# Kernel tuning notes

Hardware: AMD Instinct MI355X
Metric: run time of the kernel (lower is better)

The kernel has to match this reference:

```python
import jax, jax.numpy as jnp
import numpy as np

N = 50000   # nodes
E = 600000  # directed edges
B = 128     # graphs
IN = 128
H = 128
K = 30      # sort-pool k
C_OUT = 32
KER = 5
OUT_DIM = 10
L_OUT = K - KER + 1  # 26


def setup_inputs() -> dict:
    key = jax.random.key(0)
    ks = jax.random.split(key, 12)
    s = 0.05
    return {
        "x": jax.random.normal(ks[0], (N, IN), jnp.float32),
        "edge_index": jax.random.randint(ks[1], (2, E), 0, N),
        "batch": jnp.sort(jax.random.randint(ks[2], (N,), 0, B)),
        "W0": jax.random.normal(ks[3], (IN, H), jnp.float32) * s,
        "b0": jnp.zeros((H,), jnp.float32),
        "W1": jax.random.normal(ks[4], (H, H), jnp.float32) * s,
        "b1": jnp.zeros((H,), jnp.float32),
        "W2": jax.random.normal(ks[5], (H, H), jnp.float32) * s,
        "b2": jnp.zeros((H,), jnp.float32),
        "conv_w": jax.random.normal(ks[6], (C_OUT, H, KER), jnp.float32) * s,
        "conv_b": jnp.zeros((C_OUT,), jnp.float32),
        "lin1_w": jax.random.normal(ks[7], (C_OUT * L_OUT, H), jnp.float32) * s,
        "lin1_b": jnp.zeros((H,), jnp.float32),
        "lin2_w": jax.random.normal(ks[8], (H, OUT_DIM), jnp.float32) * s,
        "lin2_b": jnp.zeros((OUT_DIM,), jnp.float32),
    }


def reference(x, edge_index, batch, W0, b0, W1, b1, W2, b2,
              conv_w, conv_b, lin1_w, lin1_b, lin2_w, lin2_b):
    # --- GCN normalization (A + I, symmetric deg^-1/2) ---
    loops = jnp.arange(N)
    row = jnp.concatenate([edge_index[0], loops])  # source
    col = jnp.concatenate([edge_index[1], loops])  # target (aggregation side)
    deg = jax.ops.segment_sum(jnp.ones_like(col, dtype=x.dtype), col, num_segments=N)
    dinv = jax.lax.rsqrt(jnp.maximum(deg, 1.0))
    norm = dinv[row] * dinv[col]  # [E+N]

    def gcn(h, W, b):
        hw = h @ W                                            # [N,H]
        msg = hw[row] * norm[:, None]                         # gather [E+N,H]
        return jax.ops.segment_sum(msg, col, num_segments=N) + b

    h = jax.nn.relu(gcn(x, W0, b0))
    h = jax.nn.relu(gcn(h, W1, b1))
    h = jax.nn.relu(gcn(h, W2, b2))

    # --- SortAggregation: per-graph sort by last channel (desc), top-K, zero-pad ---
    last = h[:, -1]
    order = jnp.lexsort((-last, batch))  # primary: batch, secondary: last desc
    hs = h[order]
    bs = batch[order]
    counts = jax.ops.segment_sum(jnp.ones((N,), jnp.int32), batch, num_segments=B)
    starts = jnp.cumsum(counts) - counts  # exclusive prefix sum
    rank = jnp.arange(N) - starts[bs]     # within-graph rank after sort
    r = jnp.where(rank < K, rank, K)      # overflow bucket K is discarded
    pooled = jnp.zeros((B, K + 1, H), h.dtype).at[bs, r].add(hs)[:, :K]  # [B,K,H]

    # --- conv1d head (NCH layout, matches torch view/transpose) ---
    xc = jnp.transpose(pooled, (0, 2, 1))  # [B,H,K]
    y = jax.lax.conv_general_dilated(xc, conv_w, (1,), "VALID",
                                     dimension_numbers=("NCH", "OIH", "NCH"))
    y = jax.nn.relu(y + conv_b[None, :, None])  # [B,C_OUT,L_OUT]
    y = y.reshape(B, -1)
    y = jax.nn.relu(y @ lin1_w + lin1_b)
    return y @ lin2_w + lin2_b  # [B,OUT_DIM]
```

## Files before the change

kernel.cpp:

```cpp
#include <hip/hip_runtime.h>
#include <math.h>

#define Nn 50000
#define Ee 600000
#define Bg 128
#define Hd 128
#define Kt 30
#define CO 32
#define KW 5
#define LOUT 26
#define CAP 2048
#define SCB 196
#define MMB 782

typedef float v2f __attribute__((ext_vector_type(2)));
typedef short bf16x8 __attribute__((ext_vector_type(8)));
typedef float f32x4 __attribute__((ext_vector_type(4)));

__device__ __forceinline__ unsigned short bfr(float v) {
    unsigned u = __builtin_bit_cast(unsigned, v);
    unsigned r = (u + 0x7FFFu + ((u >> 16) & 1u)) >> 16;
    return (unsigned short)r;
}
__device__ __forceinline__ float bff(unsigned short h) {
    unsigned u = ((unsigned)h) << 16;
    return __builtin_bit_cast(float, u);
}

__global__ void countpack_kernel(const int* __restrict__ ei, const int* __restrict__ batch,
                            int* __restrict__ deg_i, int* __restrict__ bstart,
                            const float* __restrict__ conv_w, float* __restrict__ wT2,
                            const float* __restrict__ W0, const float* __restrict__ W1,
                            const float* __restrict__ W2,
                            ushort* __restrict__ Bph, ushort* __restrict__ Bpm,
                            ushort* __restrict__ Bpl) {
    int i = blockIdx.x * 256 + threadIdx.x;
    if (i < Ee) atomicAdd(&deg_i[ei[Ee + i]], 1);
    if (i < Nn) {
        int b = batch[i];
        if (i == 0) bstart[b] = 0;
        else if (batch[i - 1] != b) bstart[b] = i;
    }
    if (i == 0) bstart[Bg] = Nn;
    if (i < CO * KW * Hd) {
        int ci = i & 127;
        int r = i >> 7;
        int o = r / KW, k = r - o * KW;
        wT2[i] = conv_w[((size_t)o * Hd + ci) * KW + k];
    }
    if (i < 3 * 2048) {
        int l = i >> 11;
        int r = i & 2047;
        int kc = r >> 9;
        int n = (r >> 6) & 7;
        int lane = r & 63;
        int m = lane & 15, kq = lane >> 4;
        const float* W = (l == 0) ? W0 : (l == 1) ? W1 : W2;
        int col = n * 16 + m;
        size_t off = ((size_t)l * 2048 + (size_t)((kc * 8 + n) * 64 + lane)) * 8;
#pragma unroll
        for (int j = 0; j < 8; ++j) {
            float v = W[(size_t)(kc * 32 + kq * 8 + j) * Hd + col];
            unsigned short h = bfr(v);
            float r1 = v - bff(h);
            unsigned short mid = bfr(r1);
            Bph[off + j] = h;
            Bpm[off + j] = mid;
            Bpl[off + j] = bfr(r1 - bff(mid));
        }
    }
}

__global__ __launch_bounds__(256) void scanBC2_kernel(const int* __restrict__ deg_i,
                            int* __restrict__ row_ptr, float* __restrict__ dinv,
                            int* __restrict__ bstart) {
    __shared__ int ls[256];
    __shared__ int boffS;
    int tid = threadIdx.x;
    int b = blockIdx.x;
    int s = 0;
    for (int k = 0; k < b; ++k)
        s += deg_i[k * 256 + tid] + 1;
    ls[tid] = s;
    __syncthreads();
    for (int off = 128; off > 0; off >>= 1) {
        if (tid < off) ls[tid] += ls[tid + off];
        __syncthreads();
    }
    if (tid == 0) boffS = ls[0];
    __syncthreads();
    int boff = boffS;
    int i = b * 256 + tid;
    int v2 = 0;
    if (i < Nn) {
        int raw = deg_i[i];
        v2 = raw + 1;
        dinv[i] = 1.0f / sqrtf((float)(raw + 2));
    }
    ls[tid] = v2;
    __syncthreads();
    for (int off = 1; off < 256; off <<= 1) {
        int t = (tid >= off) ? ls[tid - off] : 0;
        __syncthreads();
        ls[tid] += t;
        __syncthreads();
    }
    if (i < Nn) row_ptr[i + 1] = ls[tid] + boff;
    if (i == 0) row_ptr[0] = 0;
    if (b == 0 && tid == 0) {
        for (int bb = Bg - 1; bb >= 0; --bb)
            if (bstart[bb] == -1) bstart[bb] = bstart[bb + 1];
    }
}

__device__ __forceinline__ void mmx_body(int bid, int tid,
                            const float* __restrict__ Hin,
                            const ushort* __restrict__ Bph, const ushort* __restrict__ Bpm,
                            const ushort* __restrict__ Bpl,
                            const float* __restrict__ dinv, float* __restrict__ hw) {
    int w = tid >> 6, lane = tid & 63;
    int m = lane & 15, kq = lane >> 4;
    int rowA = bid * 64 + w * 16 + m;
    bool va = rowA < Nn;
    const float* ap = Hin + (size_t)rowA * Hd;
    f32x4 acc[8];
#pragma unroll
    for (int n = 0; n < 8; ++n) acc[n] = (f32x4)0.f;
#pragma unroll
    for (int kc = 0; kc < 4; ++kc) {
        bf16x8 a0 = (bf16x8)0, a1 = (bf16x8)0, a2 = (bf16x8)0;
        if (va) {
            float av[8];
            *(float4*)&av[0] = *(const float4*)(ap + kc * 32 + kq * 8);
            *(float4*)&av[4] = *(const float4*)(ap + kc * 32 + kq * 8 + 4);
#pragma unroll
            for (int j = 0; j < 8; ++j) {
                unsigned short h = bfr(av[j]);
                float r1 = av[j] - bff(h);
                unsigned short mid = bfr(r1);
                a0[j] = (short)h;
                a1[j] = (short)mid;
                a2[j] = (short)bfr(r1 - bff(mid));
            }
        }
        const ushort* bhp = Bph + (size_t)((kc * 8) * 64 + lane) * 8;
        const ushort* bmp = Bpm + (size_t)((kc * 8) * 64 + lane) * 8;
        const ushort* blp = Bpl + (size_t)((kc * 8) * 64 + lane) * 8;
#pragma unroll
        for (int n = 0; n < 8; ++n) {
            bf16x8 b0 = *(const bf16x8*)(bhp + (size_t)n * 64 * 8);
            bf16x8 b1 = *(const bf16x8*)(bmp + (size_t)n * 64 * 8);
            bf16x8 b2 = *(const bf16x8*)(blp + (size_t)n * 64 * 8);
            acc[n] = __builtin_amdgcn_mfma_f32_16x16x32_bf16(a0, b0, acc[n], 0, 0, 0);
            acc[n] = __builtin_amdgcn_mfma_f32_16x16x32_bf16(a1, b0, acc[n], 0, 0, 0);
            acc[n] = __builtin_amdgcn_mfma_f32_16x16x32_bf16(a0, b1, acc[n], 0, 0, 0);
            acc[n] = __builtin_amdgcn_mfma_f32_16x16x32_bf16(a1, b1, acc[n], 0, 0, 0);
            acc[n] = __builtin_amdgcn_mfma_f32_16x16x32_bf16(a2, b0, acc[n], 0, 0, 0);
            acc[n] = __builtin_amdgcn_mfma_f32_16x16x32_bf16(a0, b2, acc[n], 0, 0, 0);
        }
    }
    int rbase = bid * 64 + w * 16 + kq * 4;
#pragma unroll
    for (int reg = 0; reg < 4; ++reg) {
        int r = rbase + reg;
        if (r < Nn) {
            float s = dinv[r];
#pragma unroll
            for (int n = 0; n < 8; ++n)
                hw[(size_t)r * Hd + n * 16 + m] = acc[n][reg] * s;
        }
    }
}

__global__ __launch_bounds__(256) void mmx_kernel(const float* __restrict__ Hin,
                            const ushort* __restrict__ Bph, const ushort* __restrict__ Bpm,
                            const ushort* __restrict__ Bpl,
                            const float* __restrict__ dinv, float* __restrict__ hw) {
    mmx_body(blockIdx.x, threadIdx.x, Hin, Bph, Bpm, Bpl, dinv, hw);
}

__global__ __launch_bounds__(256) void mmxfill_kernel(const float* __restrict__ Hin,
                            const ushort* __restrict__ Bph, const ushort* __restrict__ Bpm,
                            const ushort* __restrict__ Bpl,
                            const float* __restrict__ dinv, float* __restrict__ hw,
                            const int* __restrict__ ei, const int* __restrict__ row_ptr,
                            int* __restrict__ cnt, int* __restrict__ csr_src) {
    if (blockIdx.x < MMB) {
        mmx_body(blockIdx.x, threadIdx.x, Hin, Bph, Bpm, Bpl, dinv, hw);
    } else {
        int e = (blockIdx.x - MMB) * 256 + threadIdx.x;
        if (e < Ee) {
            int c = ei[Ee + e];
            int r = ei[e];
            int p = row_ptr[c] + atomicAdd(&cnt[c], 1) + 1;
            csr_src[p] = r;
        }
    }
}

__global__ __launch_bounds__(256) void agg_kernel(const float* __restrict__ hw,
                            const int* __restrict__ row_ptr, const int* __restrict__ csr_src,
                            const float* __restrict__ dinv, const float* __restrict__ bias,
                            float* __restrict__ hout) {
    int node = blockIdx.x * 4 + (threadIdx.x >> 6);
    if (node >= Nn) return;
    int lane = threadIdx.x & 63;
    const v2f* hw2 = (const v2f*)hw;
    v2f a0 = hw2[(size_t)node * 64 + lane];
    v2f a1 = 0.f, a2 = 0.f, a3 = 0.f;
    v2f a4 = 0.f, a5 = 0.f, a6 = 0.f, a7 = 0.f;
    int e0 = row_ptr[node], e1 = row_ptr[node + 1];
    int e = e0;
    for (; e + 7 < e1; e += 8) {
        int s0 = __builtin_nontemporal_load(csr_src + e);
        int s1 = __builtin_nontemporal_load(csr_src + e + 1);
        int s2 = __builtin_nontemporal_load(csr_src + e + 2);
        int s3 = __builtin_nontemporal_load(csr_src + e + 3);
        int s4 = __builtin_nontemporal_load(csr_src + e + 4);
        int s5 = __builtin_nontemporal_load(csr_src + e + 5);
        int s6 = __builtin_nontemporal_load(csr_src + e + 6);
        int s7 = __builtin_nontemporal_load(csr_src + e + 7);
        a0 += hw2[(size_t)s0 * 64 + lane];
        a1 += hw2[(size_t)s1 * 64 + lane];
        a2 += hw2[(size_t)s2 * 64 + lane];
        a3 += hw2[(size_t)s3 * 64 + lane];
        a4 += hw2[(size_t)s4 * 64 + lane];
        a5 += hw2[(size_t)s5 * 64 + lane];
        a6 += hw2[(size_t)s6 * 64 + lane];
        a7 += hw2[(size_t)s7 * 64 + lane];
    }
    if (e + 3 < e1) {
        int s0 = __builtin_nontemporal_load(csr_src + e);
        int s1 = __builtin_nontemporal_load(csr_src + e + 1);
        int s2 = __builtin_nontemporal_load(csr_src + e + 2);
        int s3 = __builtin_nontemporal_load(csr_src + e + 3);
        a4 += hw2[(size_t)s0 * 64 + lane];
        a5 += hw2[(size_t)s1 * 64 + lane];
        a6 += hw2[(size_t)s2 * 64 + lane];
        a7 += hw2[(size_t)s3 * 64 + lane];
        e += 4;
    }
    for (; e < e1; ++e) {
        int s0 = __builtin_nontemporal_load(csr_src + e);
        a0 += hw2[(size_t)s0 * 64 + lane];
    }
    v2f acc = ((a0 + a1) + (a2 + a3)) + ((a4 + a5) + (a6 + a7));
    float d = dinv[node];
    v2f bv = ((const v2f*)bias)[lane];
    v2f o;
    o.x = fmaxf(fmaf(d, acc.x, bv.x), 0.f);
    o.y = fmaxf(fmaf(d, acc.y, bv.y), 0.f);
    ((v2f*)hout)[(size_t)node * 64 + lane] = o;
}

__global__ __launch_bounds__(1024) void tail_kernel(const float* __restrict__ h,
                            const int* __restrict__ bstart,
                            const float* __restrict__ wT2, const float* __restrict__ conv_b,
                            const float* __restrict__ l1w, const float* __restrict__ l1b,
                            const float* __restrict__ l2w, const float* __restrict__ l2b,
                            float* __restrict__ out) {
    __shared__ float vals[CAP];
    __shared__ float xcl[Kt][130];
    __shared__ float fl[CO * LOUT];
    __shared__ float pz[8][Hd];
    __shared__ float z[Hd];
    __shared__ int selS[Kt];
    int b = blockIdx.x, tid = threadIdx.x;

    int s0 = bstart[b], s1 = bstart[b + 1];
    int n = s1 - s0;
    int nc = n < CAP ? n : CAP;
    if (tid < Kt) selS[tid] = -1;
    for (int j = tid; j < nc; j += 1024)
        vals[j] = h[(size_t)(s0 + j) * Hd + (Hd - 1)];
    __syncthreads();

    for (int j = tid; j < nc; j += 1024) {
        float vj = vals[j];
        int rank = 0;
        for (int i = 0; i < nc; ++i) {
            float vi = vals[i];
            rank += (vi > vj || (vi == vj && i < j)) ? 1 : 0;
        }
        if (rank < Kt) selS[rank] = s0 + j;
    }
    __syncthreads();

    for (int i = tid; i < Kt * Hd; i += 1024) {
        int t = i >> 7, c = i & 127;
        int s = selS[t];
        xcl[t][c] = (s >= 0) ? h[(size_t)s * Hd + c] : 0.f;
    }
    __syncthreads();
    if (tid < CO * LOUT) {
        int o = tid / LOUT, t = tid - o * LOUT;
        float acc = conv_b[o];
#pragma unroll
        for (int k = 0; k < KW; ++k) {
            const float* xr = &xcl[t + k][0];
            const float* wr = wT2 + ((size_t)o * KW + k) * Hd;
#pragma unroll 8
            for (int c4 = 0; c4 < 32; ++c4) {
                float2 xa = *(const float2*)(xr + c4 * 4);
                float2 xb = *(const float2*)(xr + c4 * 4 + 2);
                float4 wv = *(const float4*)(wr + c4 * 4);
                acc = fmaf(xa.x, wv.x, acc);
                acc = fmaf(xa.y, wv.y, acc);
                acc = fmaf(xb.x, wv.z, acc);
                acc = fmaf(xb.y, wv.w, acc);
            }
        }
        fl[tid] = fmaxf(acc, 0.f);
    }
    __syncthreads();
    int hh = tid & 127, chunk = tid >> 7;
    int m0 = chunk * 104;
    float acc = 0.f;
    const float* lw = l1w + (size_t)m0 * Hd + hh;
#pragma unroll 8
    for (int m = 0; m < 104; ++m)
        acc = fmaf(fl[m0 + m], lw[(size_t)m * Hd], acc);
    pz[chunk][hh] = acc;
    __syncthreads();
    if (tid < Hd) {
        float a = l1b[tid];
#pragma unroll
        for (int q = 0; q < 8; ++q) a += pz[q][tid];
        z[tid] = fmaxf(a, 0.f);
    }
    __syncthreads();
    if (tid < 10) {
        float a2 = l2b[tid];
        for (int j = 0; j < Hd; ++j)
            a2 = fmaf(z[j], l2w[j * 10 + tid], a2);
        out[b * 10 + tid] = a2;
    }
}

extern "C" void kernel_launch(void* const* d_in, const int* in_sizes, int n_in,
                              void* d_out, int out_size, void* d_ws, size_t ws_size,
                              hipStream_t stream) {
    const float* x      = (const float*)d_in[0];
    const int*   ei     = (const int*)d_in[1];
    const int*   batch  = (const int*)d_in[2];
    const float* W0     = (const float*)d_in[3];
    const float* b0     = (const float*)d_in[4];
    const float* W1     = (const float*)d_in[5];
    const float* b1     = (const float*)d_in[6];
    const float* W2     = (const float*)d_in[7];
    const float* b2     = (const float*)d_in[8];
    const float* conv_w = (const float*)d_in[9];
    const float* conv_b = (const float*)d_in[10];
    const float* l1w    = (const float*)d_in[11];
    const float* l1b    = (const float*)d_in[12];
    const float* l2w    = (const float*)d_in[13];
    const float* l2b    = (const float*)d_in[14];
    float* out = (float*)d_out;

    int* wsI = (int*)d_ws;
    size_t off = 0;
    int*   deg_i   = wsI + off; off += Nn;
    int*   cnt     = wsI + off; off += Nn;
    int*   bstart  = wsI + off; off += 132;
    int*   row_ptr = wsI + off; off += 50004;
    float* dinv    = (float*)(wsI + off); off += Nn;
    int*   csr_src = wsI + off; off += Ee;
    off = (off + 3) & ~(size_t)3;
    ushort* Bph  = (ushort*)(wsI + off); off += 3 * 16384 / 2;
    ushort* Bpm  = (ushort*)(wsI + off); off += 3 * 16384 / 2;
    ushort* Bpl  = (ushort*)(wsI + off); off += 3 * 16384 / 2;
    float* hw    = (float*)(wsI + off); off += (size_t)Nn * Hd;
    float* hbuf  = (float*)(wsI + off); off += (size_t)Nn * Hd;
    float* wT2   = (float*)(wsI + off); off += CO * KW * Hd;

    hipMemsetAsync(deg_i, 0xFF, (size_t)(Nn + Nn + 132) * 4, stream);
    countpack_kernel<<<(Ee + 255) / 256, 256, 0, stream>>>(ei, batch, deg_i, bstart,
        conv_w, wT2, W0, W1, W2, Bph, Bpm, Bpl);
    scanBC2_kernel<<<SCB, 256, 0, stream>>>(deg_i, row_ptr, dinv, bstart);
    dim3 aggGrid((Nn + 3) / 4);
    mmxfill_kernel<<<MMB + (Ee + 255) / 256, 256, 0, stream>>>(x, Bph, Bpm, Bpl,
        dinv, hw, ei, row_ptr, cnt, csr_src);
    agg_kernel<<<aggGrid, 256, 0, stream>>>(hw, row_ptr, csr_src, dinv, b0, hbuf);
    mmx_kernel<<<MMB, 256, 0, stream>>>(hbuf, Bph + 16384, Bpm + 16384, Bpl + 16384, dinv, hw);
    agg_kernel<<<aggGrid, 256, 0, stream>>>(hw, row_ptr, csr_src, dinv, b1, hbuf);
    mmx_kernel<<<MMB, 256, 0, stream>>>(hbuf, Bph + 32768, Bpm + 32768, Bpl + 32768, dinv, hw);
    agg_kernel<<<aggGrid, 256, 0, stream>>>(hw, row_ptr, csr_src, dinv, b2, hbuf);
    tail_kernel<<<Bg, 1024, 0, stream>>>(hbuf, bstart, wT2, conv_b,
                                         l1w, l1b, l2w, l2b, out);
}
```

Baseline: 443.3 us.

## Compute only last channel for all nodes, full aggregation only for top-K

The final full-width aggregation over all nodes is replaced by a lightweight kernel that aggregates only channel 127, which is the sort key. The tail kernel then runs the full 128-channel aggregation only for the 30 selected nodes per graph. This avoids gathering and writing the whole N×H tensor for the last layer. In exchange, the last-column gather is strided (one float per 512-byte row, so poor coalescing) and the tail does serial per-node aggregation. Results must match those of the old full aggregation for both ranking and features.

```diff
diff --git a/kernel.cpp b/kernel.cpp
--- a/kernel.cpp
+++ b/kernel.cpp
@@ -253,8 +253,57 @@
     ((v2f*)hout)[(size_t)node * 64 + lane] = o;
 }
 
-__global__ __launch_bounds__(1024) void tail_kernel(const float* __restrict__ h,
-                            const int* __restrict__ bstart,
+__global__ __launch_bounds__(256) void lastcol_kernel(const float* __restrict__ hw,
+                            const int* __restrict__ row_ptr, const int* __restrict__ csr_src,
+                            const float* __restrict__ dinv, const float* __restrict__ b2,
+                            float* __restrict__ lastv) {
+    int node = blockIdx.x * 256 + threadIdx.x;
+    if (node >= Nn) return;
+    float a0 = hw[(size_t)node * Hd + 127];
+    float a1 = 0.f, a2 = 0.f, a3 = 0.f, a4 = 0.f, a5 = 0.f, a6 = 0.f, a7 = 0.f;
+    int e0 = row_ptr[node], e1 = row_ptr[node + 1];
+    int e = e0;
+    for (; e + 7 < e1; e += 8) {
+        int s0 = __builtin_nontemporal_load(csr_src + e);
+        int s1 = __builtin_nontemporal_load(csr_src + e + 1);
+        int s2 = __builtin_nontemporal_load(csr_src + e + 2);
+        int s3 = __builtin_nontemporal_load(csr_src + e + 3);
+        int s4 = __builtin_nontemporal_load(csr_src + e + 4);
+        int s5 = __builtin_nontemporal_load(csr_src + e + 5);
+        int s6 = __builtin_nontemporal_load(csr_src + e + 6);
+        int s7 = __builtin_nontemporal_load(csr_src + e + 7);
+        a0 += hw[(size_t)s0 * Hd + 127];
+        a1 += hw[(size_t)s1 * Hd + 127];
+        a2 += hw[(size_t)s2 * Hd + 127];
+        a3 += hw[(size_t)s3 * Hd + 127];
+        a4 += hw[(size_t)s4 * Hd + 127];
+        a5 += hw[(size_t)s5 * Hd + 127];
+        a6 += hw[(size_t)s6 * Hd + 127];
+        a7 += hw[(size_t)s7 * Hd + 127];
+    }
+    if (e + 3 < e1) {
+        int s0 = __builtin_nontemporal_load(csr_src + e);
+        int s1 = __builtin_nontemporal_load(csr_src + e + 1);
+        int s2 = __builtin_nontemporal_load(csr_src + e + 2);
+        int s3 = __builtin_nontemporal_load(csr_src + e + 3);
+        a4 += hw[(size_t)s0 * Hd + 127];
+        a5 += hw[(size_t)s1 * Hd + 127];
+        a6 += hw[(size_t)s2 * Hd + 127];
+        a7 += hw[(size_t)s3 * Hd + 127];
+        e += 4;
+    }
+    for (; e < e1; ++e) {
+        int s0 = __builtin_nontemporal_load(csr_src + e);
+        a0 += hw[(size_t)s0 * Hd + 127];
+    }
+    float acc = ((a0 + a1) + (a2 + a3)) + ((a4 + a5) + (a6 + a7));
+    lastv[node] = fmaxf(fmaf(dinv[node], acc, b2[127]), 0.f);
+}
+
+__global__ __launch_bounds__(1024) void tail_kernel(const float* __restrict__ hw,
+                            const int* __restrict__ bstart, const int* __restrict__ row_ptr,
+                            const int* __restrict__ csr_src, const float* __restrict__ dinv,
+                            const float* __restrict__ b2, const float* __restrict__ lastv,
                             const float* __restrict__ wT2, const float* __restrict__ conv_b,
                             const float* __restrict__ l1w, const float* __restrict__ l1b,
                             const float* __restrict__ l2w, const float* __restrict__ l2b,
@@ -272,7 +321,7 @@
     int nc = n < CAP ? n : CAP;
     if (tid < Kt) selS[tid] = -1;
     for (int j = tid; j < nc; j += 1024)
-        vals[j] = h[(size_t)(s0 + j) * Hd + (Hd - 1)];
+        vals[j] = lastv[s0 + j];
     __syncthreads();
 
     for (int j = tid; j < nc; j += 1024) {
@@ -286,10 +335,58 @@
     }
     __syncthreads();
 
-    for (int i = tid; i < Kt * Hd; i += 1024) {
-        int t = i >> 7, c = i & 127;
+    int wv = tid >> 6, lane = tid & 63;
+    const v2f* hw2 = (const v2f*)hw;
+    v2f bv = ((const v2f*)b2)[lane];
+    for (int t = wv; t < Kt; t += 16) {
         int s = selS[t];
-        xcl[t][c] = (s >= 0) ? h[(size_t)s * Hd + c] : 0.f;
+        v2f o = (v2f)0.f;
+        if (s >= 0) {
+            v2f a0 = hw2[(size_t)s * 64 + lane];
+            v2f a1 = 0.f, a2 = 0.f, a3 = 0.f;
+            v2f a4 = 0.f, a5 = 0.f, a6 = 0.f, a7 = 0.f;
+            int e0 = row_ptr[s], e1 = row_ptr[s + 1];
+            int e = e0;
+            for (; e + 7 < e1; e += 8) {
+                int q0 = __builtin_nontemporal_load(csr_src + e);
+                int q1 = __builtin_nontemporal_load(csr_src + e + 1);
+                int q2 = __builtin_nontemporal_load(csr_src + e + 2);
+                int q3 = __builtin_nontemporal_load(csr_src + e + 3);
+                int q4 = __builtin_nontemporal_load(csr_src + e + 4);
+                int q5 = __builtin_nontemporal_load(csr_src + e + 5);
+                int q6 = __builtin_nontemporal_load(csr_src + e + 6);
+                int q7 = __builtin_nontemporal_load(csr_src + e + 7);
+                a0 += hw2[(size_t)q0 * 64 + lane];
+                a1 += hw2[(size_t)q1 * 64 + lane];
+                a2 += hw2[(size_t)q2 * 64 + lane];
+                a3 += hw2[(size_t)q3 * 64 + lane];
+                a4 += hw2[(size_t)q4 * 64 + lane];
+                a5 += hw2[(size_t)q5 * 64 + lane];
+                a6 += hw2[(size_t)q6 * 64 + lane];
+                a7 += hw2[(size_t)q7 * 64 + lane];
+            }
+            if (e + 3 < e1) {
+                int q0 = __builtin_nontemporal_load(csr_src + e);
+                int q1 = __builtin_nontemporal_load(csr_src + e + 1);
+                int q2 = __builtin_nontemporal_load(csr_src + e + 2);
+                int q3 = __builtin_nontemporal_load(csr_src + e + 3);
+                a4 += hw2[(size_t)q0 * 64 + lane];
+                a5 += hw2[(size_t)q1 * 64 + lane];
+                a6 += hw2[(size_t)q2 * 64 + lane];
+                a7 += hw2[(size_t)q3 * 64 + lane];
+                e += 4;
+            }
+            for (; e < e1; ++e) {
+                int q0 = __builtin_nontemporal_load(csr_src + e);
+                a0 += hw2[(size_t)q0 * 64 + lane];
+            }
+            v2f acc = ((a0 + a1) + (a2 + a3)) + ((a4 + a5) + (a6 + a7));
+            float d = dinv[s];
+            o.x = fmaxf(fmaf(d, acc.x, bv.x), 0.f);
+            o.y = fmaxf(fmaf(d, acc.y, bv.y), 0.f);
+        }
+        xcl[t][lane * 2] = o.x;
+        xcl[t][lane * 2 + 1] = o.y;
     }
     __syncthreads();
     if (tid < CO * LOUT) {
@@ -303,11 +400,11 @@
             for (int c4 = 0; c4 < 32; ++c4) {
                 float2 xa = *(const float2*)(xr + c4 * 4);
                 float2 xb = *(const float2*)(xr + c4 * 4 + 2);
-                float4 wv = *(const float4*)(wr + c4 * 4);
-                acc = fmaf(xa.x, wv.x, acc);
-                acc = fmaf(xa.y, wv.y, acc);
-                acc = fmaf(xb.x, wv.z, acc);
-                acc = fmaf(xb.y, wv.w, acc);
+                float4 wv2 = *(const float4*)(wr + c4 * 4);
+                acc = fmaf(xa.x, wv2.x, acc);
+                acc = fmaf(xa.y, wv2.y, acc);
+                acc = fmaf(xb.x, wv2.z, acc);
+                acc = fmaf(xb.y, wv2.w, acc);
             }
         }
         fl[tid] = fmaxf(acc, 0.f);
@@ -372,6 +469,7 @@
     float* hw    = (float*)(wsI + off); off += (size_t)Nn * Hd;
     float* hbuf  = (float*)(wsI + off); off += (size_t)Nn * Hd;
     float* wT2   = (float*)(wsI + off); off += CO * KW * Hd;
+    float* lastv = (float*)(wsI + off); off += Nn;
 
     hipMemsetAsync(deg_i, 0xFF, (size_t)(Nn + Nn + 132) * 4, stream);
     countpack_kernel<<<(Ee + 255) / 256, 256, 0, stream>>>(ei, batch, deg_i, bstart,
@@ -384,7 +482,7 @@
     mmx_kernel<<<MMB, 256, 0, stream>>>(hbuf, Bph + 16384, Bpm + 16384, Bpl + 16384, dinv, hw);
     agg_kernel<<<aggGrid, 256, 0, stream>>>(hw, row_ptr, csr_src, dinv, b1, hbuf);
     mmx_kernel<<<MMB, 256, 0, stream>>>(hbuf, Bph + 32768, Bpm + 32768, Bpl + 32768, dinv, hw);
-    agg_kernel<<<aggGrid, 256, 0, stream>>>(hw, row_ptr, csr_src, dinv, b2, hbuf);
-    tail_kernel<<<Bg, 1024, 0, stream>>>(hbuf, bstart, wT2, conv_b,
-                                         l1w, l1b, l2w, l2b, out);
-}
+    lastcol_kernel<<<(Nn + 255) / 256, 256, 0, stream>>>(hw, row_ptr, csr_src, dinv, b2, lastv);
+    tail_kernel<<<Bg, 1024, 0, stream>>>(hw, bstart, row_ptr, csr_src, dinv, b2, lastv,
+                                         wT2, conv_b, l1w, l1b, l2w, l2b, out);
+}
```

Result: faster. 403.8 us (-8.9%).
